# Performance work log

Measured on AMD Instinct MI355X. Metric: run time of the kernel, lower is better.

## Reference

```python
import jax, jax.numpy as jnp
import numpy as np

CH = 256            # channels
IN_C = CH // 2      # 128
INTER_C = CH // 16  # 16
NUM_POINTS = 32
BN_EPS = 1e-5


def conv1x1(x, W, b=None):
    # x: [B,C,H,W], W: [O,C]
    y = jnp.einsum('oc,bchw->bohw', W, x)
    if b is not None:
        y = y + b[None, :, None, None]
    return y


def bilinear_sample(feat, sx, sy):
    """feat [B,C,H,W]; sx,sy [B,N,P] continuous index coords; border padding."""
    B, C, H, W = feat.shape
    x0f = jnp.floor(sx)
    y0f = jnp.floor(sy)
    wx = sx - x0f
    wy = sy - y0f
    x0 = jnp.clip(x0f.astype(jnp.int32), 0, W - 1)
    x1 = jnp.clip(x0f.astype(jnp.int32) + 1, 0, W - 1)
    y0 = jnp.clip(y0f.astype(jnp.int32), 0, H - 1)
    y1 = jnp.clip(y0f.astype(jnp.int32) + 1, 0, H - 1)
    feat_f = feat.reshape(B, C, H * W).transpose(0, 2, 1)  # [B,HW,C]

    def gather(yi, xi):
        idx = (yi * W + xi).reshape(B, -1)  # [B,N*P]
        return jnp.take_along_axis(feat_f, idx[:, :, None], axis=1)  # [B,N*P,C]

    wxf = wx.reshape(B, -1, 1)
    wyf = wy.reshape(B, -1, 1)
    out = (gather(y0, x0) * (1 - wxf) * (1 - wyf)
           + gather(y0, x1) * wxf * (1 - wyf)
           + gather(y1, x0) * (1 - wxf) * wyf
           + gather(y1, x1) * wxf * wyf)
    N, P = sx.shape[1], sx.shape[2]
    return out.reshape(B, N, P, C)


def multi_scale_attention(qf, vf, Wq, bq, Wk, bk, Wv, bv, Woff, boff):
    # deformable-style point-sampling attention with NUM_POINTS samples per query
    B, _, H, W = qf.shape
    N = H * W
    q = conv1x1(qf, Wq, bq).reshape(B, INTER_C, N).transpose(0, 2, 1)  # [B,N,Ci]
    k = conv1x1(vf, Wk, bk)                                            # [B,Ci,H,W]
    v = conv1x1(vf, Wv, bv)                                            # [B,Cv,H,W]
    off = conv1x1(qf, Woff, boff).reshape(B, NUM_POINTS, 2, N)
    off = off.transpose(0, 3, 1, 2)                                    # [B,N,P,2] (dx,dy)
    ys, xs = jnp.meshgrid(jnp.arange(H, dtype=qf.dtype),
                          jnp.arange(W, dtype=qf.dtype), indexing='ij')
    sx = xs.reshape(-1)[None, :, None] + off[..., 0]                   # [B,N,P]
    sy = ys.reshape(-1)[None, :, None] + off[..., 1]
    k_s = bilinear_sample(k, sx, sy)                                   # [B,N,P,Ci]
    v_s = bilinear_sample(v, sx, sy)                                   # [B,N,P,Cv]
    logits = jnp.einsum('bnc,bnpc->bnp', q, k_s) / jnp.sqrt(jnp.asarray(INTER_C, qf.dtype))
    attn = jax.nn.softmax(logits, axis=-1)
    out = jnp.einsum('bnp,bnpc->bnc', attn, v_s)                       # [B,N,Cv]
    return out.transpose(0, 2, 1).reshape(B, -1, H, W)


def setup_inputs() -> dict:
    key = jax.random.key(0)
    ks = jax.random.split(key, 12)
    B, Hl, Wl, Hh, Wh = 2, 64, 64, 32, 32
    s = 0.02
    return {
        'low_feature': jax.random.normal(ks[0], (B, CH, Hl, Wl), jnp.float32),
        'high_feature': jax.random.normal(ks[1], (B, CH, Hh, Wh), jnp.float32),
        'W1': jax.random.normal(ks[2], (IN_C, 2 * CH), jnp.float32) * s,
        'b1': jnp.zeros((IN_C,), jnp.float32),
        'W2': jax.random.normal(ks[3], (IN_C, CH), jnp.float32) * s,
        'b2': jnp.zeros((IN_C,), jnp.float32),
        'Wq': jax.random.normal(ks[4], (INTER_C, IN_C), jnp.float32) * s,
        'bq': jnp.zeros((INTER_C,), jnp.float32),
        'Wk': jax.random.normal(ks[5], (INTER_C, IN_C), jnp.float32) * s,
        'bk': jnp.zeros((INTER_C,), jnp.float32),
        'Wv': jax.random.normal(ks[6], (IN_C, IN_C), jnp.float32) * s,
        'bv': jnp.zeros((IN_C,), jnp.float32),
        'Woff': jax.random.normal(ks[7], (2 * NUM_POINTS, IN_C), jnp.float32) * 0.5,
        'boff': jnp.zeros((2 * NUM_POINTS,), jnp.float32),
        'Wb': jax.random.normal(ks[8], (CH, IN_C + CH), jnp.float32) * s,
        'gamma': jnp.ones((CH,), jnp.float32),
        'beta': jnp.zeros((CH,), jnp.float32),
        'rmean': jnp.zeros((CH,), jnp.float32),
        'rvar': jnp.ones((CH,), jnp.float32),
    }


def reference(low_feature, high_feature, W1, b1, W2, b2, Wq, bq, Wk, bk,
              Wv, bv, Woff, boff, Wb, gamma, beta, rmean, rvar):
    B, _, Hl, Wl = low_feature.shape
    # F.interpolate(mode='bilinear', align_corners=False) == jax.image half-pixel bilinear
    high_up = jax.image.resize(high_feature, (B, CH, Hl, Wl), method='bilinear')
    query_feature = conv1x1(jnp.concatenate([high_up, low_feature], axis=1), W1, b1)
    value_feature = conv1x1(high_up, W2, b2)
    value_feature = multi_scale_attention(query_feature, value_feature,
                                          Wq, bq, Wk, bk, Wv, bv, Woff, boff)
    x = conv1x1(jnp.concatenate([value_feature, high_up], axis=1), Wb)
    # BatchNorm (eval form) + ReLU
    x = (x - rmean[None, :, None, None]) * jax.lax.rsqrt(rvar + BN_EPS)[None, :, None, None]
    x = x * gamma[None, :, None, None] + beta[None, :, None, None]
    return jax.nn.relu(x)
```

## Files before the change

### kernel.cpp

```cpp
#include <hip/hip_runtime.h>
#include <hip/hip_bf16.h>

#define NL 4096
#define HH 32
#define WH 32

typedef __attribute__((ext_vector_type(8))) short s8v;
typedef __attribute__((ext_vector_type(4))) short s4v;
typedef __attribute__((ext_vector_type(4))) float f32x4;

static __device__ inline unsigned short f2bf(float x) {
  __hip_bfloat16 h = __float2bfloat16(x);
  return *reinterpret_cast<unsigned short*>(&h);
}
static __device__ inline float bfbits2f(unsigned int lo16) {
  unsigned int u = lo16 << 16;
  return *reinterpret_cast<float*>(&u);
}
static __device__ inline int swizzle_wg(int b) {
  return ((b & 7) << 6) | (b >> 3);
}

__global__ __launch_bounds__(256) void convert_weights_k(
    const float* __restrict__ w1, const float* __restrict__ w2,
    const float* __restrict__ wq, const float* __restrict__ woff,
    const float* __restrict__ wk, const float* __restrict__ wv,
    const float* __restrict__ wb, short* __restrict__ dst) {
  int i = (blockIdx.x * 256 + threadIdx.x) * 4;
  const float* src; int off;
  if      (i <  65536) { src = w1;   off = 0; }
  else if (i <  98304) { src = w2;   off = 65536; }
  else if (i < 100352) { src = wq;   off = 98304; }
  else if (i < 108544) { src = woff; off = 100352; }
  else if (i < 110592) { src = wk;   off = 108544; }
  else if (i < 126976) { src = wv;   off = 110592; }
  else if (i < 225280) { src = wb;   off = 126976; }
  else return;
  float4 v = *(const float4*)(src + (i - off));
  s4v o;
  o[0] = (short)f2bf(v.x); o[1] = (short)f2bf(v.y);
  o[2] = (short)f2bf(v.z); o[3] = (short)f2bf(v.w);
  *(s4v*)(dst + i) = o;
}

__global__ __launch_bounds__(512, 4) void k1_fused(
    const float* __restrict__ low, const float* __restrict__ high,
    const short* __restrict__ wc,
    const float* __restrict__ b1, const float* __restrict__ b2,
    const float* __restrict__ bq, const float* __restrict__ boff,
    const float* __restrict__ bk, const float* __restrict__ bv,
    short* __restrict__ xh, float* __restrict__ q_t, float* __restrict__ k_t,
    float* __restrict__ off_t, short* __restrict__ v_t) {
  __shared__ short xin_s[16 * 520];
  __shared__ short qf_s[16 * 136];
  __shared__ short vf_s[16 * 136];
  __shared__ float hrow_s[256][2][11];
  const int tid = threadIdx.x;
  const int wg = swizzle_wg(blockIdx.x);
  const int pix0 = wg * 16;
  const int b = pix0 >> 12;
  const int n0 = pix0 & (NL - 1);

  const int yrow = n0 >> 6;
  const int x0blk = n0 & 63;
  const int xc0 = (x0blk >> 1) - 1;

  float syf = yrow * 0.5f - 0.25f;
  float y0f = floorf(syf);
  float wy = syf - y0f;
  int y0i = (int)y0f;
  int y0c = min(HH - 1, max(0, y0i)), y1c = min(HH - 1, max(0, y0i + 1));

  const int nl = tid & 15, cg = tid >> 4;
  const int n = n0 + nl;
  float lo_reg[8];
#pragma unroll
  for (int i = 0; i < 8; i++)
    lo_reg[i] = low[(size_t)(b * 256 + cg * 8 + i) * NL + n];

  {
    const int c = tid >> 1, r = tid & 1;
    const int yr = r ? y1c : y0c;
    const float* src = high + ((size_t)(b * 256 + c) * HH + yr) * WH;
#pragma unroll
    for (int j = 0; j < 10; j++) {
      int col = min(WH - 1, max(0, xc0 + j));
      hrow_s[c][r][j] = src[col];
    }
  }
  __syncthreads();

  {
    const int x = x0blk + nl;
    float sxf = x * 0.5f - 0.25f;
    float x0f_ = floorf(sxf);
    float wx = sxf - x0f_;
    int x0i = (int)x0f_;
    int j0 = min(WH - 1, max(0, x0i)) - xc0;
    int j1 = min(WH - 1, max(0, x0i + 1)) - xc0;
    float w1x = 1.f - wx;
#pragma unroll
    for (int i = 0; i < 8; i++) {
      int c = cg * 8 + i;
      float top = hrow_s[c][0][j0] * w1x + hrow_s[c][0][j1] * wx;
      float bot = hrow_s[c][1][j0] * w1x + hrow_s[c][1][j1] * wx;
      float v = top * (1.f - wy) + bot * wy;
      xin_s[nl * 520 + c] = (short)f2bf(v);
      xin_s[nl * 520 + 256 + c] = (short)f2bf(lo_reg[i]);
    }
  }
  __syncthreads();

  {
    const int r = tid >> 5, c0 = (tid & 31) * 8;
    s8v v0 = *(const s8v*)(xin_s + r * 520 + c0);
    *(s8v*)(xh + (size_t)(pix0 + r) * 256 + c0) = v0;
  }

  const int wave = tid >> 6, lane = tid & 63;
  const int quad = lane >> 4, id = lane & 15;

  {
    f32x4 acc = (f32x4){0.f, 0.f, 0.f, 0.f};
    const short* a0 = wc + (size_t)(wave * 16 + id) * 512 + quad * 8;
    const short* bp = xin_s + id * 520 + quad * 8;
#pragma unroll
    for (int kk = 0; kk < 512; kk += 32)
      acc = __builtin_amdgcn_mfma_f32_16x16x32_bf16(
          *(const s8v*)(a0 + kk), *(const s8v*)(bp + kk), acc, 0, 0, 0);
    int m0 = wave * 16 + quad * 4;
    s4v o0;
#pragma unroll
    for (int r = 0; r < 4; r++) o0[r] = (short)f2bf(acc[r] + b1[m0 + r]);
    *(s4v*)(qf_s + id * 136 + m0) = o0;
  }

  {
    f32x4 acc = (f32x4){0.f, 0.f, 0.f, 0.f};
    const short* a0 = wc + 65536 + (size_t)(wave * 16 + id) * 256 + quad * 8;
    const short* bp = xin_s + id * 520 + quad * 8;
#pragma unroll
    for (int kk = 0; kk < 256; kk += 32)
      acc = __builtin_amdgcn_mfma_f32_16x16x32_bf16(
          *(const s8v*)(a0 + kk), *(const s8v*)(bp + kk), acc, 0, 0, 0);
    int m0 = wave * 16 + quad * 4;
    s4v o0;
#pragma unroll
    for (int r = 0; r < 4; r++) o0[r] = (short)f2bf(acc[r] + b2[m0 + r]);
    *(s4v*)(vf_s + id * 136 + m0) = o0;
  }
  __syncthreads();

  for (int f = wave; f < 14; f += 8) {
    const short* ap = wc + 98304 + (size_t)(f * 16 + id) * 128 + quad * 8;
    const short* bp = (f < 5 ? qf_s : vf_s) + id * 136 + quad * 8;
    f32x4 acc = (f32x4){0.f, 0.f, 0.f, 0.f};
#pragma unroll
    for (int kk = 0; kk < 128; kk += 32)
      acc = __builtin_amdgcn_mfma_f32_16x16x32_bf16(
          *(const s8v*)(ap + kk), *(const s8v*)(bp + kk), acc, 0, 0, 0);
    const int pix = pix0 + id;
    const int mq = quad * 4;
    if (f == 0) {
      f32x4 v;
#pragma unroll
      for (int r = 0; r < 4; r++) v[r] = acc[r] + bq[mq + r];
      *(f32x4*)(q_t + (size_t)pix * 16 + mq) = v;
    } else if (f < 5) {
      int m = (f - 1) * 16 + mq;
      f32x4 v;
#pragma unroll
      for (int r = 0; r < 4; r++) v[r] = acc[r] + boff[m + r];
      *(f32x4*)(off_t + (size_t)pix * 64 + m) = v;
    } else if (f == 5) {
      f32x4 v;
#pragma unroll
      for (int r = 0; r < 4; r++) v[r] = acc[r] + bk[mq + r];
      *(f32x4*)(k_t + (size_t)pix * 16 + mq) = v;
    } else {
      int m = (f - 6) * 16 + mq;
      s4v o;
#pragma unroll
      for (int r = 0; r < 4; r++) o[r] = (short)f2bf(acc[r] + bv[m + r]);
      *(s4v*)(v_t + (size_t)pix * 128 + m) = o;
    }
  }
}

__global__ __launch_bounds__(512, 8) void k2_fused(
    const float* __restrict__ q_t, const float* __restrict__ k_t,
    const short* __restrict__ v_t, const float* __restrict__ off_t,
    const short* __restrict__ xh, const short* __restrict__ wb,
    const float* __restrict__ gamma, const float* __restrict__ beta,
    const float* __restrict__ rmean, const float* __restrict__ rvar,
    float* __restrict__ out) {
  __shared__ float2 s_wi[16][32][4];
  __shared__ short attn_s[16 * 136];
  __shared__ short xh_s[16][264];
  const int tid = threadIdx.x;
  const int wave = tid >> 6, lane = tid & 63;
  const int wg = swizzle_wg(blockIdx.x);
  const int pix0 = wg * 16;

  const int sp = tid >> 5, sc = (tid & 31) * 8;
  uint4 xh_reg = *(const uint4*)(xh + (size_t)(pix0 + sp) * 256 + sc);

  for (int qi = 0; qi < 2; qi++) {
    const int ql = wave * 2 + qi;
    const int qidx = pix0 + ql;
    const int b = qidx >> 12;
    const int n = qidx & (NL - 1);
    const int qy = n >> 6, qx = n & 63;

    const int pt = lane >> 1, h = lane & 1;
    float2 dxy = *(const float2*)(off_t + (size_t)qidx * 64 + 2 * pt);

    const float* qp = q_t + (size_t)qidx * 16;
    float qreg[16];
#pragma unroll
    for (int i = 0; i < 16; i += 4) {
      float4 t4 = *(const float4*)(qp + i);
      qreg[i] = t4.x; qreg[i + 1] = t4.y; qreg[i + 2] = t4.z; qreg[i + 3] = t4.w;
    }

    float sx = (float)qx + dxy.x;
    float sy = (float)qy + dxy.y;
    float x0f = floorf(sx), y0f = floorf(sy);
    float wx = sx - x0f, wy = sy - y0f;
    int x0i = (int)x0f, y0i = (int)y0f;
    int x0 = min(63, max(0, x0i)), x1 = min(63, max(0, x0i + 1));
    int y0 = min(63, max(0, y0i)), y1 = min(63, max(0, y0i + 1));

    int   yr  = h ? y1 : y0;
    float wyr = h ? wy : (1.f - wy);
    int   pa = yr * 64 + x0, pb = yr * 64 + x1;
    float wa = wyr * (1.f - wx), wb_ = wyr * wx;

    const float* kb = k_t + (size_t)b * NL * 16;
    float da = 0.f, db = 0.f;
    {
      const float* ka = kb + (size_t)pa * 16;
      const float* kc = kb + (size_t)pb * 16;
#pragma unroll
      for (int i = 0; i < 16; i += 4) {
        float4 a4 = *(const float4*)(ka + i);
        float4 c4 = *(const float4*)(kc + i);
        da = fmaf(qreg[i], a4.x, da); da = fmaf(qreg[i + 1], a4.y, da);
        da = fmaf(qreg[i + 2], a4.z, da); da = fmaf(qreg[i + 3], a4.w, da);
        db = fmaf(qreg[i], c4.x, db); db = fmaf(qreg[i + 1], c4.y, db);
        db = fmaf(qreg[i + 2], c4.z, db); db = fmaf(qreg[i + 3], c4.w, db);
      }
    }
    float part = wa * da + wb_ * db;
    part += __shfl_xor(part, 1, 64);
    float logit = part * 0.25f;

    float e = __expf(logit);

    s_wi[ql][pt][2 * h + 0] = make_float2(e * wa,  __int_as_float(pa << 7));
    s_wi[ql][pt][2 * h + 1] = make_float2(e * wb_, __int_as_float(pb << 7));

    const int t = lane >> 4, chunk = lane & 15;
    const short* vb = v_t + (size_t)b * NL * 128 + chunk * 8;
    float o[8];
#pragma unroll
    for (int j = 0; j < 8; j++) o[j] = 0.f;
    for (int base = 0; base < 32; base += 8) {
      float w8[8]; int ix[8];
#pragma unroll
      for (int j = 0; j < 8; j++) {
        float2 wi = s_wi[ql][base + j][t];
        w8[j] = wi.x;
        ix[j] = __float_as_int(wi.y);
      }
      uint4 u[8];
#pragma unroll
      for (int j = 0; j < 8; j++) u[j] = *(const uint4*)(vb + ix[j]);
#pragma unroll
      for (int j = 0; j < 8; j++) {
        o[0] = fmaf(w8[j], bfbits2f(u[j].x & 0xffffu), o[0]);
        o[1] = fmaf(w8[j], bfbits2f(u[j].x >> 16),     o[1]);
        o[2] = fmaf(w8[j], bfbits2f(u[j].y & 0xffffu), o[2]);
        o[3] = fmaf(w8[j], bfbits2f(u[j].y >> 16),     o[3]);
        o[4] = fmaf(w8[j], bfbits2f(u[j].z & 0xffffu), o[4]);
        o[5] = fmaf(w8[j], bfbits2f(u[j].z >> 16),     o[5]);
        o[6] = fmaf(w8[j], bfbits2f(u[j].w & 0xffffu), o[6]);
        o[7] = fmaf(w8[j], bfbits2f(u[j].w >> 16),     o[7]);
      }
    }
    float ssum = e;
#pragma unroll
    for (int s = 32; s > 0; s >>= 1) ssum += __shfl_xor(ssum, s, 64);
    float scale = 2.f / ssum;

#pragma unroll
    for (int j = 0; j < 8; j++) {
      o[j] += __shfl_xor(o[j], 16, 64);
      o[j] += __shfl_xor(o[j], 32, 64);
    }
    if (t == 0) {
      uint4 pk;
      pk.x = (unsigned)f2bf(o[0] * scale) | ((unsigned)f2bf(o[1] * scale) << 16);
      pk.y = (unsigned)f2bf(o[2] * scale) | ((unsigned)f2bf(o[3] * scale) << 16);
      pk.z = (unsigned)f2bf(o[4] * scale) | ((unsigned)f2bf(o[5] * scale) << 16);
      pk.w = (unsigned)f2bf(o[6] * scale) | ((unsigned)f2bf(o[7] * scale) << 16);
      *(uint4*)(attn_s + ql * 136 + chunk * 8) = pk;
    }
  }
  *(uint4*)(&xh_s[sp][sc]) = xh_reg;
  __syncthreads();

  {
    const int quad = lane >> 4, id = lane & 15;
    const int pix = pix0 + id;
    const short* bs = attn_s + id * 136 + quad * 8;
    const short* bg = &xh_s[id][quad * 8];
    const int bb = pix >> 12, nlow = pix & (NL - 1);
#pragma unroll
    for (int j = 0; j < 2; j++) {
      const int m0 = wave * 16 + j * 128;
      f32x4 acc = (f32x4){0.f, 0.f, 0.f, 0.f};
      const short* ap = wb + (size_t)(m0 + id) * 384 + quad * 8;
#pragma unroll
      for (int k = 0; k < 4; k++)
        acc = __builtin_amdgcn_mfma_f32_16x16x32_bf16(
            *(const s8v*)(ap + k * 32), *(const s8v*)(bs + k * 32), acc, 0, 0, 0);
#pragma unroll
      for (int k = 0; k < 8; k++)
        acc = __builtin_amdgcn_mfma_f32_16x16x32_bf16(
            *(const s8v*)(ap + 128 + k * 32), *(const s8v*)(bg + k * 32), acc, 0, 0, 0);

      const int mbase = m0 + quad * 4;
#pragma unroll
      for (int r = 0; r < 4; r++) {
        int o = mbase + r;
        float s  = gamma[o] * rsqrtf(rvar[o] + 1e-5f);
        float sh = beta[o] - rmean[o] * s;
        __builtin_nontemporal_store(fmaxf(fmaf(acc[r], s, sh), 0.f),
                                    &out[((size_t)bb * 256 + o) * NL + nlow]);
      }
    }
  }
}

extern "C" void kernel_launch(void* const* d_in, const int* in_sizes, int n_in,
                              void* d_out, int out_size, void* d_ws, size_t ws_size,
                              hipStream_t stream) {
  const float* low   = (const float*)d_in[0];
  const float* high  = (const float*)d_in[1];
  const float* W1    = (const float*)d_in[2];
  const float* b1    = (const float*)d_in[3];
  const float* W2    = (const float*)d_in[4];
  const float* b2    = (const float*)d_in[5];
  const float* Wq    = (const float*)d_in[6];
  const float* bq    = (const float*)d_in[7];
  const float* Wk    = (const float*)d_in[8];
  const float* bk    = (const float*)d_in[9];
  const float* Wv    = (const float*)d_in[10];
  const float* bv    = (const float*)d_in[11];
  const float* Woff  = (const float*)d_in[12];
  const float* boff  = (const float*)d_in[13];
  const float* Wb    = (const float*)d_in[14];
  const float* gamma = (const float*)d_in[15];
  const float* beta  = (const float*)d_in[16];
  const float* rmean = (const float*)d_in[17];
  const float* rvar  = (const float*)d_in[18];
  float* out = (float*)d_out;

  short* ws    = (short*)d_ws;
  short* xh    = ws;
  short* v_t   = xh + 2097152;
  short* wc    = v_t + 1048576;
  float* q_t   = (float*)(wc + 225280);
  float* k_t   = q_t + 131072;
  float* off_t = k_t + 131072;

  convert_weights_k<<<880, 256, 0, stream>>>(W1, W2, Wq, Woff, Wk, Wv, Wb, wc);
  k1_fused<<<512, 512, 0, stream>>>(low, high, wc, b1, b2, bq, boff, bk, bv,
                                    xh, q_t, k_t, off_t, v_t);
  k2_fused<<<512, 512, 0, stream>>>(q_t, k_t, v_t, off_t, xh, wc + 126976,
                                    gamma, beta, rmean, rvar, out);
}
```

Before: 152.5 us.

## Double per-workgroup pixel tile to 32 and reuse weight fragments across two MFMAs

```diff
diff --git a/kernel.cpp b/kernel.cpp
--- a/kernel.cpp
+++ b/kernel.cpp
@@ -17,8 +17,8 @@
   unsigned int u = lo16 << 16;
   return *reinterpret_cast<float*>(&u);
 }
-static __device__ inline int swizzle_wg(int b) {
-  return ((b & 7) << 6) | (b >> 3);
+static __device__ inline int swizzle_wg32(int b) {
+  return ((b & 7) << 5) | (b >> 3);
 }
 
 __global__ __launch_bounds__(256) void convert_weights_k(
@@ -43,7 +43,7 @@
   *(s4v*)(dst + i) = o;
 }
 
-__global__ __launch_bounds__(512, 4) void k1_fused(
+__global__ __launch_bounds__(512, 2) void k1_fused(
     const float* __restrict__ low, const float* __restrict__ high,
     const short* __restrict__ wc,
     const float* __restrict__ b1, const float* __restrict__ b2,
@@ -51,19 +51,19 @@
     const float* __restrict__ bk, const float* __restrict__ bv,
     short* __restrict__ xh, float* __restrict__ q_t, float* __restrict__ k_t,
     float* __restrict__ off_t, short* __restrict__ v_t) {
-  __shared__ short xin_s[16 * 520];
-  __shared__ short qf_s[16 * 136];
-  __shared__ short vf_s[16 * 136];
-  __shared__ float hrow_s[256][2][11];
+  __shared__ __align__(16) char smem[33280 + 22528];
+  short* xin_s = (short*)smem;
+  float* hrow_s = (float*)(smem + 33280);
+  short* qf_s = (short*)(smem + 33280);
+  short* vf_s = (short*)(smem + 33280 + 8704);
+
   const int tid = threadIdx.x;
-  const int wg = swizzle_wg(blockIdx.x);
-  const int pix0 = wg * 16;
+  const int wg = swizzle_wg32(blockIdx.x);
+  const int pix0 = wg * 32;
   const int b = pix0 >> 12;
   const int n0 = pix0 & (NL - 1);
-
   const int yrow = n0 >> 6;
   const int x0blk = n0 & 63;
-  const int xc0 = (x0blk >> 1) - 1;
 
   float syf = yrow * 0.5f - 0.25f;
   float y0f = floorf(syf);
@@ -71,142 +71,185 @@
   int y0i = (int)y0f;
   int y0c = min(HH - 1, max(0, y0i)), y1c = min(HH - 1, max(0, y0i + 1));
 
-  const int nl = tid & 15, cg = tid >> 4;
-  const int n = n0 + nl;
-  float lo_reg[8];
-#pragma unroll
-  for (int i = 0; i < 8; i++)
-    lo_reg[i] = low[(size_t)(b * 256 + cg * 8 + i) * NL + n];
+  for (int tt = 0; tt < 2; tt++) {
+    const int pt0 = tt * 16;
+    const int xsub = x0blk + pt0;
+    const int xc0 = (xsub >> 1) - 1;
+    const int nsub = n0 + pt0;
+
+    const int cL = tid >> 1, hL = tid & 1;
+    const float* lp = low + (size_t)(b * 256 + cL) * NL + nsub + hL * 8;
+    float4 lo0 = *(const float4*)(lp);
+    float4 lo1 = *(const float4*)(lp + 4);
+
+    if (tt) __syncthreads();
+    {
+      const int c = tid >> 1, r = tid & 1;
+      const int yr = r ? y1c : y0c;
+      const float* src = high + ((size_t)(b * 256 + c) * HH + yr) * WH;
+      float* hd = hrow_s + (c * 2 + r) * 11;
+#pragma unroll
+      for (int j = 0; j < 10; j++) {
+        int col = min(WH - 1, max(0, xc0 + j));
+        hd[j] = src[col];
+      }
+    }
+    __syncthreads();
+
+    {
+      const int nl = tid & 15, cg = tid >> 4;
+      const int x = xsub + nl;
+      float sxf = x * 0.5f - 0.25f;
+      float x0f_ = floorf(sxf);
+      float wx = sxf - x0f_;
+      int x0i = (int)x0f_;
+      int j0 = min(WH - 1, max(0, x0i)) - xc0;
+      int j1 = min(WH - 1, max(0, x0i + 1)) - xc0;
+      float w1x = 1.f - wx;
+#pragma unroll
+      for (int i = 0; i < 8; i++) {
+        int c = cg * 8 + i;
+        const float* hr = hrow_s + c * 22;
+        float top = hr[j0] * w1x + hr[j1] * wx;
+        float bot = hr[11 + j0] * w1x + hr[11 + j1] * wx;
+        float v = top * (1.f - wy) + bot * wy;
+        xin_s[(pt0 + nl) * 520 + c] = (short)f2bf(v);
+      }
+      float lv[8] = {lo0.x, lo0.y, lo0.z, lo0.w, lo1.x, lo1.y, lo1.z, lo1.w};
+#pragma unroll
+      for (int p = 0; p < 8; p++)
+        xin_s[(pt0 + hL * 8 + p) * 520 + 256 + cL] = (short)f2bf(lv[p]);
+    }
+  }
+  __syncthreads();
 
   {
-    const int c = tid >> 1, r = tid & 1;
-    const int yr = r ? y1c : y0c;
-    const float* src = high + ((size_t)(b * 256 + c) * HH + yr) * WH;
-#pragma unroll
-    for (int j = 0; j < 10; j++) {
-      int col = min(WH - 1, max(0, xc0 + j));
-      hrow_s[c][r][j] = src[col];
-    }
-  }
-  __syncthreads();
-
-  {
-    const int x = x0blk + nl;
-    float sxf = x * 0.5f - 0.25f;
-    float x0f_ = floorf(sxf);
-    float wx = sxf - x0f_;
-    int x0i = (int)x0f_;
-    int j0 = min(WH - 1, max(0, x0i)) - xc0;
-    int j1 = min(WH - 1, max(0, x0i + 1)) - xc0;
-    float w1x = 1.f - wx;
-#pragma unroll
-    for (int i = 0; i < 8; i++) {
-      int c = cg * 8 + i;
-      float top = hrow_s[c][0][j0] * w1x + hrow_s[c][0][j1] * wx;
-      float bot = hrow_s[c][1][j0] * w1x + hrow_s[c][1][j1] * wx;
-      float v = top * (1.f - wy) + bot * wy;
-      xin_s[nl * 520 + c] = (short)f2bf(v);
-      xin_s[nl * 520 + 256 + c] = (short)f2bf(lo_reg[i]);
-    }
-  }
-  __syncthreads();
-
-  {
-    const int r = tid >> 5, c0 = (tid & 31) * 8;
+    const int r = tid >> 4, c0 = (tid & 15) * 16;
     s8v v0 = *(const s8v*)(xin_s + r * 520 + c0);
+    s8v v1 = *(const s8v*)(xin_s + r * 520 + c0 + 8);
     *(s8v*)(xh + (size_t)(pix0 + r) * 256 + c0) = v0;
+    *(s8v*)(xh + (size_t)(pix0 + r) * 256 + c0 + 8) = v1;
   }
 
   const int wave = tid >> 6, lane = tid & 63;
   const int quad = lane >> 4, id = lane & 15;
 
   {
-    f32x4 acc = (f32x4){0.f, 0.f, 0.f, 0.f};
+    f32x4 acc0 = (f32x4){0.f, 0.f, 0.f, 0.f};
+    f32x4 acc1 = (f32x4){0.f, 0.f, 0.f, 0.f};
     const short* a0 = wc + (size_t)(wave * 16 + id) * 512 + quad * 8;
-    const short* bp = xin_s + id * 520 + quad * 8;
-#pragma unroll
-    for (int kk = 0; kk < 512; kk += 32)
-      acc = __builtin_amdgcn_mfma_f32_16x16x32_bf16(
-          *(const s8v*)(a0 + kk), *(const s8v*)(bp + kk), acc, 0, 0, 0);
+    const short* bp0 = xin_s + id * 520 + quad * 8;
+    const short* bp1 = bp0 + 16 * 520;
+#pragma unroll
+    for (int kk = 0; kk < 512; kk += 32) {
+      s8v af = *(const s8v*)(a0 + kk);
+      acc0 = __builtin_amdgcn_mfma_f32_16x16x32_bf16(af, *(const s8v*)(bp0 + kk), acc0, 0, 0, 0);
+      acc1 = __builtin_amdgcn_mfma_f32_16x16x32_bf16(af, *(const s8v*)(bp1 + kk), acc1, 0, 0, 0);
+    }
     int m0 = wave * 16 + quad * 4;
-    s4v o0;
-#pragma unroll
-    for (int r = 0; r < 4; r++) o0[r] = (short)f2bf(acc[r] + b1[m0 + r]);
+    s4v o0, o1;
+#pragma unroll
+    for (int r = 0; r < 4; r++) {
+      o0[r] = (short)f2bf(acc0[r] + b1[m0 + r]);
+      o1[r] = (short)f2bf(acc1[r] + b1[m0 + r]);
+    }
     *(s4v*)(qf_s + id * 136 + m0) = o0;
+    *(s4v*)(qf_s + (16 + id) * 136 + m0) = o1;
   }
 
   {
-    f32x4 acc = (f32x4){0.f, 0.f, 0.f, 0.f};
+    f32x4 acc0 = (f32x4){0.f, 0.f, 0.f, 0.f};
+    f32x4 acc1 = (f32x4){0.f, 0.f, 0.f, 0.f};
     const short* a0 = wc + 65536 + (size_t)(wave * 16 + id) * 256 + quad * 8;
-    const short* bp = xin_s + id * 520 + quad * 8;
-#pragma unroll
-    for (int kk = 0; kk < 256; kk += 32)
-      acc = __builtin_amdgcn_mfma_f32_16x16x32_bf16(
-          *(const s8v*)(a0 + kk), *(const s8v*)(bp + kk), acc, 0, 0, 0);
+    const short* bp0 = xin_s + id * 520 + quad * 8;
+    const short* bp1 = bp0 + 16 * 520;
+#pragma unroll
+    for (int kk = 0; kk < 256; kk += 32) {
+      s8v af = *(const s8v*)(a0 + kk);
+      acc0 = __builtin_amdgcn_mfma_f32_16x16x32_bf16(af, *(const s8v*)(bp0 + kk), acc0, 0, 0, 0);
+      acc1 = __builtin_amdgcn_mfma_f32_16x16x32_bf16(af, *(const s8v*)(bp1 + kk), acc1, 0, 0, 0);
+    }
     int m0 = wave * 16 + quad * 4;
-    s4v o0;
-#pragma unroll
-    for (int r = 0; r < 4; r++) o0[r] = (short)f2bf(acc[r] + b2[m0 + r]);
+    s4v o0, o1;
+#pragma unroll
+    for (int r = 0; r < 4; r++) {
+      o0[r] = (short)f2bf(acc0[r] + b2[m0 + r]);
+      o1[r] = (short)f2bf(acc1[r] + b2[m0 + r]);
+    }
     *(s4v*)(vf_s + id * 136 + m0) = o0;
+    *(s4v*)(vf_s + (16 + id) * 136 + m0) = o1;
   }
   __syncthreads();
 
   for (int f = wave; f < 14; f += 8) {
     const short* ap = wc + 98304 + (size_t)(f * 16 + id) * 128 + quad * 8;
-    const short* bp = (f < 5 ? qf_s : vf_s) + id * 136 + quad * 8;
-    f32x4 acc = (f32x4){0.f, 0.f, 0.f, 0.f};
-#pragma unroll
-    for (int kk = 0; kk < 128; kk += 32)
-      acc = __builtin_amdgcn_mfma_f32_16x16x32_bf16(
-          *(const s8v*)(ap + kk), *(const s8v*)(bp + kk), acc, 0, 0, 0);
-    const int pix = pix0 + id;
+    const short* base = (f < 5 ? qf_s : vf_s);
+    const short* bp0 = base + id * 136 + quad * 8;
+    const short* bp1 = base + (16 + id) * 136 + quad * 8;
+    f32x4 acc0 = (f32x4){0.f, 0.f, 0.f, 0.f};
+    f32x4 acc1 = (f32x4){0.f, 0.f, 0.f, 0.f};
+#pragma unroll
+    for (int kk = 0; kk < 128; kk += 32) {
+      s8v af = *(const s8v*)(ap + kk);
+      acc0 = __builtin_amdgcn_mfma_f32_16x16x32_bf16(af, *(const s8v*)(bp0 + kk), acc0, 0, 0, 0);
+      acc1 = __builtin_amdgcn_mfma_f32_16x16x32_bf16(af, *(const s8v*)(bp1 + kk), acc1, 0, 0, 0);
+    }
     const int mq = quad * 4;
-    if (f == 0) {
-      f32x4 v;
-#pragma unroll
-      for (int r = 0; r < 4; r++) v[r] = acc[r] + bq[mq + r];
-      *(f32x4*)(q_t + (size_t)pix * 16 + mq) = v;
-    } else if (f < 5) {
-      int m = (f - 1) * 16 + mq;
-      f32x4 v;
-#pragma unroll
-      for (int r = 0; r < 4; r++) v[r] = acc[r] + boff[m + r];
-      *(f32x4*)(off_t + (size_t)pix * 64 + m) = v;
-    } else if (f == 5) {
-      f32x4 v;
-#pragma unroll
-      for (int r = 0; r < 4; r++) v[r] = acc[r] + bk[mq + r];
-      *(f32x4*)(k_t + (size_t)pix * 16 + mq) = v;
-    } else {
-      int m = (f - 6) * 16 + mq;
-      s4v o;
-#pragma unroll
-      for (int r = 0; r < 4; r++) o[r] = (short)f2bf(acc[r] + bv[m + r]);
-      *(s4v*)(v_t + (size_t)pix * 128 + m) = o;
-    }
-  }
-}
-
-__global__ __launch_bounds__(512, 8) void k2_fused(
+#pragma unroll
+    for (int t = 0; t < 2; t++) {
+      const f32x4 acc = t ? acc1 : acc0;
+      const int pix = pix0 + t * 16 + id;
+      if (f == 0) {
+        f32x4 v;
+#pragma unroll
+        for (int r = 0; r < 4; r++) v[r] = acc[r] + bq[mq + r];
+        *(f32x4*)(q_t + (size_t)pix * 16 + mq) = v;
+      } else if (f < 5) {
+        int m = (f - 1) * 16 + mq;
+        f32x4 v;
+#pragma unroll
+        for (int r = 0; r < 4; r++) v[r] = acc[r] + boff[m + r];
+        *(f32x4*)(off_t + (size_t)pix * 64 + m) = v;
+      } else if (f == 5) {
+        f32x4 v;
+#pragma unroll
+        for (int r = 0; r < 4; r++) v[r] = acc[r] + bk[mq + r];
+        *(f32x4*)(k_t + (size_t)pix * 16 + mq) = v;
+      } else {
+        int m = (f - 6) * 16 + mq;
+        s4v o;
+#pragma unroll
+        for (int r = 0; r < 4; r++) o[r] = (short)f2bf(acc[r] + bv[m + r]);
+        *(s4v*)(v_t + (size_t)pix * 128 + m) = o;
+      }
+    }
+  }
+}
+
+__global__ __launch_bounds__(512, 2) void k2_fused(
     const float* __restrict__ q_t, const float* __restrict__ k_t,
     const short* __restrict__ v_t, const float* __restrict__ off_t,
     const short* __restrict__ xh, const short* __restrict__ wb,
     const float* __restrict__ gamma, const float* __restrict__ beta,
     const float* __restrict__ rmean, const float* __restrict__ rvar,
     float* __restrict__ out) {
-  __shared__ float2 s_wi[16][32][4];
-  __shared__ short attn_s[16 * 136];
-  __shared__ short xh_s[16][264];
+  __shared__ __align__(16) char smem[32768 + 8704 + 16896];
+  float2* s_wi = (float2*)smem;
+  short* attn_s = (short*)(smem + 32768);
+  short* xh_s = (short*)(smem + 32768 + 8704);
+
   const int tid = threadIdx.x;
   const int wave = tid >> 6, lane = tid & 63;
-  const int wg = swizzle_wg(blockIdx.x);
-  const int pix0 = wg * 16;
-
-  const int sp = tid >> 5, sc = (tid & 31) * 8;
-  uint4 xh_reg = *(const uint4*)(xh + (size_t)(pix0 + sp) * 256 + sc);
-
-  for (int qi = 0; qi < 2; qi++) {
-    const int ql = wave * 2 + qi;
+  const int wg = swizzle_wg32(blockIdx.x);
+  const int pix0 = wg * 32;
+
+  const int sp = tid >> 4, sc = (tid & 15) * 16;
+  const short* xp = xh + (size_t)(pix0 + sp) * 256 + sc;
+  uint4 xr0 = *(const uint4*)(xp);
+  uint4 xr1 = *(const uint4*)(xp + 8);
+
+  for (int qi = 0; qi < 4; qi++) {
+    const int ql = wave * 4 + qi;
     const int qidx = pix0 + ql;
     const int b = qidx >> 12;
     const int n = qidx & (NL - 1);
@@ -257,8 +300,8 @@
 
     float e = __expf(logit);
 
-    s_wi[ql][pt][2 * h + 0] = make_float2(e * wa,  __int_as_float(pa << 7));
-    s_wi[ql][pt][2 * h + 1] = make_float2(e * wb_, __int_as_float(pb << 7));
+    s_wi[(ql * 32 + pt) * 4 + 2 * h + 0] = make_float2(e * wa,  __int_as_float(pa << 7));
+    s_wi[(ql * 32 + pt) * 4 + 2 * h + 1] = make_float2(e * wb_, __int_as_float(pb << 7));
 
     const int t = lane >> 4, chunk = lane & 15;
     const short* vb = v_t + (size_t)b * NL * 128 + chunk * 8;
@@ -269,7 +312,7 @@
       float w8[8]; int ix[8];
 #pragma unroll
       for (int j = 0; j < 8; j++) {
-        float2 wi = s_wi[ql][base + j][t];
+        float2 wi = s_wi[(ql * 32 + base + j) * 4 + t];
         w8[j] = wi.x;
         ix[j] = __float_as_int(wi.y);
       }
@@ -307,37 +350,52 @@
       *(uint4*)(attn_s + ql * 136 + chunk * 8) = pk;
     }
   }
-  *(uint4*)(&xh_s[sp][sc]) = xh_reg;
+  *(uint4*)(xh_s + sp * 264 + sc) = xr0;
+  *(uint4*)(xh_s + sp * 264 + sc + 8) = xr1;
   __syncthreads();
 
   {
     const int quad = lane >> 4, id = lane & 15;
-    const int pix = pix0 + id;
-    const short* bs = attn_s + id * 136 + quad * 8;
-    const short* bg = &xh_s[id][quad * 8];
-    const int bb = pix >> 12, nlow = pix & (NL - 1);
+    const short* bs0 = attn_s + id * 136 + quad * 8;
+    const short* bs1 = attn_s + (16 + id) * 136 + quad * 8;
+    const short* bg0 = xh_s + id * 264 + quad * 8;
+    const short* bg1 = xh_s + (16 + id) * 264 + quad * 8;
 #pragma unroll
     for (int j = 0; j < 2; j++) {
       const int m0 = wave * 16 + j * 128;
-      f32x4 acc = (f32x4){0.f, 0.f, 0.f, 0.f};
       const short* ap = wb + (size_t)(m0 + id) * 384 + quad * 8;
-#pragma unroll
-      for (int k = 0; k < 4; k++)
-        acc = __builtin_amdgcn_mfma_f32_16x16x32_bf16(
-            *(const s8v*)(ap + k * 32), *(const s8v*)(bs + k * 32), acc, 0, 0, 0);
-#pragma unroll
-      for (int k = 0; k < 8; k++)
-        acc = __builtin_amdgcn_mfma_f32_16x16x32_bf16(
-            *(const s8v*)(ap + 128 + k * 32), *(const s8v*)(bg + k * 32), acc, 0, 0, 0);
-
+      f32x4 acc0 = (f32x4){0.f, 0.f, 0.f, 0.f};
+      f32x4 acc1 = (f32x4){0.f, 0.f, 0.f, 0.f};
+#pragma unroll
+      for (int k = 0; k < 4; k++) {
+        s8v af = *(const s8v*)(ap + k * 32);
+        acc0 = __builtin_amdgcn_mfma_f32_16x16x32_bf16(af, *(const s8v*)(bs0 + k * 32), acc0, 0, 0, 0);
+        acc1 = __builtin_amdgcn_mfma_f32_16x16x32_bf16(af, *(const s8v*)(bs1 + k * 32), acc1, 0, 0, 0);
+      }
+#pragma unroll
+      for (int k = 0; k < 8; k++) {
+        s8v af = *(const s8v*)(ap + 128 + k * 32);
+        acc0 = __builtin_amdgcn_mfma_f32_16x16x32_bf16(af, *(const s8v*)(bg0 + k * 32), acc0, 0, 0, 0);
+        acc1 = __builtin_amdgcn_mfma_f32_16x16x32_bf16(af, *(const s8v*)(bg1 + k * 32), acc1, 0, 0, 0);
+      }
       const int mbase = m0 + quad * 4;
 #pragma unroll
       for (int r = 0; r < 4; r++) {
         int o = mbase + r;
         float s  = gamma[o] * rsqrtf(rvar[o] + 1e-5f);
         float sh = beta[o] - rmean[o] * s;
-        __builtin_nontemporal_store(fmaxf(fmaf(acc[r], s, sh), 0.f),
-                                    &out[((size_t)bb * 256 + o) * NL + nlow]);
+        {
+          const int pix = pix0 + id;
+          const int bb = pix >> 12, nlow = pix & (NL - 1);
+          __builtin_nontemporal_store(fmaxf(fmaf(acc0[r], s, sh), 0.f),
+                                      &out[((size_t)bb * 256 + o) * NL + nlow]);
+        }
+        {
+          const int pix = pix0 + 16 + id;
+          const int bb = pix >> 12, nlow = pix & (NL - 1);
+          __builtin_nontemporal_store(fmaxf(fmaf(acc1[r], s, sh), 0.f),
+                                      &out[((size_t)bb * 256 + o) * NL + nlow]);
+        }
       }
     }
   }
@@ -375,9 +433,9 @@
   float* k_t   = q_t + 131072;
   float* off_t = k_t + 131072;
 
-  convert_weights_k<<<880, 256, 0, stream>>>(W1, W2, Wq, Woff, Wk, Wv, Wb, wc);
-  k1_fused<<<512, 512, 0, stream>>>(low, high, wc, b1, b2, bq, boff, bk, bv,
+  convert_weights_k<<<220, 256, 0, stream>>>(W1, W2, Wq, Woff, Wk, Wv, Wb, wc);
+  k1_fused<<<256, 512, 0, stream>>>(low, high, wc, b1, b2, bq, boff, bk, bv,
                                     xh, q_t, k_t, off_t, v_t);
-  k2_fused<<<512, 512, 0, stream>>>(q_t, k_t, v_t, off_t, xh, wc + 126976,
+  k2_fused<<<256, 512, 0, stream>>>(q_t, k_t, v_t, off_t, xh, wc + 126976,
                                     gamma, beta, rmean, rvar, out);
 }
```

After: 137.0 us. -10.2%, faster.
